# Optimization experiments

Hardware: AMD Instinct MI355X
Metric: run time of the kernel (lower is better)

Reference implementation:

```python
import jax, jax.numpy as jnp
import numpy as np
from jax import lax

B, T, D, H, HODE = 1024, 128, 64, 256, 256
DT = 0.1  # times spaced by 0.1 == integration_step_size -> one RK4 step per interval


def setup_inputs() -> dict:
    key = jax.random.key(0)
    ks = jax.random.split(key, 10)
    s = lambda fan: 1.0 / np.sqrt(fan)
    return {
        "x": jax.random.normal(ks[0], (B, T, D), jnp.float32),
        "times": jnp.arange(T, dtype=jnp.float32) * DT,
        "mask": (jax.random.uniform(ks[1], (B, T)) > 0.3).astype(jnp.float32),
        # ODE MLP: Linear(H->HODE), ReLU, Linear(HODE->H)
        "W1": jax.random.uniform(ks[2], (HODE, H), jnp.float32, -s(H), s(H)),
        "b1": jax.random.uniform(ks[3], (HODE,), jnp.float32, -s(H), s(H)),
        "W2": jax.random.uniform(ks[4], (H, HODE), jnp.float32, -s(HODE), s(HODE)),
        "b2": jax.random.uniform(ks[5], (H,), jnp.float32, -s(HODE), s(HODE)),
        # GRUCell params (torch layout: [3H, D]/[3H, H], gate order r,z,n)
        "W_ih": jax.random.uniform(ks[6], (3 * H, D), jnp.float32, -s(H), s(H)),
        "b_ih": jax.random.uniform(ks[7], (3 * H,), jnp.float32, -s(H), s(H)),
        "W_hh": jax.random.uniform(ks[8], (3 * H, H), jnp.float32, -s(H), s(H)),
        "b_hh": jax.random.uniform(ks[9], (3 * H,), jnp.float32, -s(H), s(H)),
    }


def _ode_gru_forward(x, times, mask, W1, b1, W2, b2, W_ih, b_ih, W_hh, b_hh):
    Bs, Ts, _ = x.shape
    Hs = W_hh.shape[1]

    def f(h):  # autonomous ODE vector field: MLP(h)
        return jnp.maximum(h @ W1.T + b1, 0.0) @ W2.T + b2

    def rk4_step(h, dt):
        k1 = f(h)
        k2 = f(h + 0.5 * dt * k1)
        k3 = f(h + 0.5 * dt * k2)
        k4 = f(h + dt * k3)
        return h + (dt / 6.0) * (k1 + 2.0 * k2 + 2.0 * k3 + k4)

    def gru_update(xt, h, m):
        gi = xt @ W_ih.T + b_ih  # [B, 3H]
        gh = h @ W_hh.T + b_hh
        i_r, i_z, i_n = jnp.split(gi, 3, axis=-1)
        h_r, h_z, h_n = jnp.split(gh, 3, axis=-1)
        r = jax.nn.sigmoid(i_r + h_r)
        z = jax.nn.sigmoid(i_z + h_z)
        n = jnp.tanh(i_n + r * h_n)
        h_next = (1.0 - z) * n + z * h
        m = m[:, None]
        return m * h_next + (1.0 - m) * h

    h0 = gru_update(x[:, 0], jnp.zeros((Bs, Hs), x.dtype), mask[:, 0])
    dts = times[1:] - times[:-1]  # [T-1]

    def step(h, inp):
        xt, mt, dt = inp
        h_ode = rk4_step(h, dt)
        h = gru_update(xt, h_ode, mt)
        return h, h

    xs = (jnp.swapaxes(x[:, 1:], 0, 1), jnp.swapaxes(mask[:, 1:], 0, 1), dts)
    _, hs = lax.scan(step, h0, xs)  # hs: [T-1, B, H]
    out = jnp.concatenate([h0[None], hs], axis=0)  # [T, B, H]
    return jnp.swapaxes(out, 0, 1)  # [B, T, H]


def reference(x, times, mask, W1, b1, W2, b2, W_ih, b_ih, W_hh, b_hh):
    return _ode_gru_forward(x, times, mask, W1, b1, W2, b2, W_ih, b_ih, W_hh, b_hh)
```

## Files before the change

kernel.cpp:

```cpp
#include <hip/hip_runtime.h>
#include <math.h>

#define BN 1024
#define TT 128
#define DD 64
#define HH 256
#define H3 768
#define BB 4

__device__ float g_W1t[HH * HH];
__device__ float g_W2t[HH * HH];
__device__ float g_Whht[HH * H3];
__device__ float g_Wiht[DD * H3];

__global__ __launch_bounds__(256) void prep_kernel(
    const float* __restrict__ W1, const float* __restrict__ W2,
    const float* __restrict__ Whh, const float* __restrict__ Wih)
{
  const int idx = blockIdx.x * blockDim.x + threadIdx.x;
  if (idx < HH * HH) {
    const int k = idx >> 8;
    const int i = idx & (HH - 1);
    g_W1t[idx] = W1[i * HH + k];
    g_W2t[idx] = W2[i * HH + k];
  }
  if (idx < HH * H3) {
    const int k = idx / H3;
    const int j = idx - k * H3;
    g_Whht[idx] = Whh[j * HH + k];
  }
  if (idx < DD * H3) {
    const int k = idx / H3;
    const int j = idx - k * H3;
    g_Wiht[idx] = Wih[j * DD + k];
  }
}

#define MV256(WT, INBUF, ACC) do {                                         \
    ACC[0] = 0.0f; ACC[1] = 0.0f; ACC[2] = 0.0f; ACC[3] = 0.0f;            \
    const float* wp_ = &(WT)[i];                                           \
    _Pragma("unroll 8")                                                    \
    for (int k_ = 0; k_ < HH; ++k_) {                                      \
      const float w_ = wp_[k_ * HH];                                       \
      const float4 hv_ = *reinterpret_cast<const float4*>(&(INBUF)[k_][0]);\
      ACC[0] = fmaf(w_, hv_.x, ACC[0]);                                    \
      ACC[1] = fmaf(w_, hv_.y, ACC[1]);                                    \
      ACC[2] = fmaf(w_, hv_.z, ACC[2]);                                    \
      ACC[3] = fmaf(w_, hv_.w, ACC[3]);                                    \
    }                                                                      \
  } while (0)

#define FEVAL(INBUF, KV) do {                                              \
    float a_[BB];                                                          \
    MV256(g_W1t, INBUF, a_);                                               \
    _Pragma("unroll")                                                      \
    for (int bb_ = 0; bb_ < BB; ++bb_)                                     \
      sh_u[i][bb_] = fmaxf(a_[bb_] + b1i, 0.0f);                           \
    __syncthreads();                                                       \
    MV256(g_W2t, sh_u, a_);                                                \
    _Pragma("unroll")                                                      \
    for (int bb_ = 0; bb_ < BB; ++bb_) KV[bb_] = a_[bb_] + b2i;            \
  } while (0)

__global__ __launch_bounds__(256) void odegru_kernel(
    const float* __restrict__ x, const float* __restrict__ times,
    const float* __restrict__ mask,
    const float* __restrict__ b1, const float* __restrict__ b2,
    const float* __restrict__ bih, const float* __restrict__ bhh,
    float* __restrict__ out)
{
  const int i = threadIdx.x;
  const int bbase = blockIdx.x * BB;

  __shared__ __align__(16) float sh_h[HH][BB];
  __shared__ __align__(16) float sh_in[HH][BB];
  __shared__ __align__(16) float sh_u[HH][BB];
  __shared__ __align__(16) float sh_x[DD][BB];

  const float b1i = b1[i];
  const float b2i = b2[i];
  const float bihr = bih[i], bihz = bih[i + HH], bihn = bih[i + 2 * HH];
  const float bhhr = bhh[i], bhhz = bhh[i + HH], bhhn = bhh[i + 2 * HH];

#pragma unroll
  for (int bb = 0; bb < BB; ++bb) sh_h[i][bb] = 0.0f;

  for (int t = 0; t < TT; ++t) {
    {
      const int bb = i >> 6, d = i & 63;
      sh_x[d][bb] = x[((size_t)(bbase + bb) * TT + t) * DD + d];
    }
    if (t == 0) {
#pragma unroll
      for (int bb = 0; bb < BB; ++bb) sh_in[i][bb] = 0.0f;
    }
    __syncthreads();

    if (t > 0) {
      const float dt = times[t] - times[t - 1];
      float kv[BB], ks[BB];

      FEVAL(sh_h, kv);
#pragma unroll
      for (int bb = 0; bb < BB; ++bb) {
        ks[bb] = kv[bb];
        sh_in[i][bb] = sh_h[i][bb] + 0.5f * dt * kv[bb];
      }
      __syncthreads();
      FEVAL(sh_in, kv);
#pragma unroll
      for (int bb = 0; bb < BB; ++bb) {
        ks[bb] += 2.0f * kv[bb];
        sh_in[i][bb] = sh_h[i][bb] + 0.5f * dt * kv[bb];
      }
      __syncthreads();
      FEVAL(sh_in, kv);
#pragma unroll
      for (int bb = 0; bb < BB; ++bb) {
        ks[bb] += 2.0f * kv[bb];
        sh_in[i][bb] = sh_h[i][bb] + dt * kv[bb];
      }
      __syncthreads();
      FEVAL(sh_in, kv);
#pragma unroll
      for (int bb = 0; bb < BB; ++bb) {
        ks[bb] += kv[bb];
        sh_in[i][bb] = sh_h[i][bb] + (dt * (1.0f / 6.0f)) * ks[bb];
      }
      __syncthreads();
    }

    float racc[BB], zacc[BB], ghn[BB], gin[BB];
#pragma unroll
    for (int bb = 0; bb < BB; ++bb) {
      racc[bb] = bihr + bhhr;
      zacc[bb] = bihz + bhhz;
      ghn[bb] = bhhn;
      gin[bb] = bihn;
    }

    {
      const float* wp = &g_Whht[i];
#pragma unroll 4
      for (int k = 0; k < HH; ++k) {
        const float4 hv = *reinterpret_cast<const float4*>(&sh_in[k][0]);
        const float wr = wp[k * H3];
        const float wz = wp[k * H3 + HH];
        const float wn = wp[k * H3 + 2 * HH];
        racc[0] = fmaf(wr, hv.x, racc[0]); racc[1] = fmaf(wr, hv.y, racc[1]);
        racc[2] = fmaf(wr, hv.z, racc[2]); racc[3] = fmaf(wr, hv.w, racc[3]);
        zacc[0] = fmaf(wz, hv.x, zacc[0]); zacc[1] = fmaf(wz, hv.y, zacc[1]);
        zacc[2] = fmaf(wz, hv.z, zacc[2]); zacc[3] = fmaf(wz, hv.w, zacc[3]);
        ghn[0] = fmaf(wn, hv.x, ghn[0]); ghn[1] = fmaf(wn, hv.y, ghn[1]);
        ghn[2] = fmaf(wn, hv.z, ghn[2]); ghn[3] = fmaf(wn, hv.w, ghn[3]);
      }
    }
    {
      const float* wp = &g_Wiht[i];
#pragma unroll 4
      for (int k = 0; k < DD; ++k) {
        const float4 xv = *reinterpret_cast<const float4*>(&sh_x[k][0]);
        const float wr = wp[k * H3];
        const float wz = wp[k * H3 + HH];
        const float wn = wp[k * H3 + 2 * HH];
        racc[0] = fmaf(wr, xv.x, racc[0]); racc[1] = fmaf(wr, xv.y, racc[1]);
        racc[2] = fmaf(wr, xv.z, racc[2]); racc[3] = fmaf(wr, xv.w, racc[3]);
        zacc[0] = fmaf(wz, xv.x, zacc[0]); zacc[1] = fmaf(wz, xv.y, zacc[1]);
        zacc[2] = fmaf(wz, xv.z, zacc[2]); zacc[3] = fmaf(wz, xv.w, zacc[3]);
        gin[0] = fmaf(wn, xv.x, gin[0]); gin[1] = fmaf(wn, xv.y, gin[1]);
        gin[2] = fmaf(wn, xv.z, gin[2]); gin[3] = fmaf(wn, xv.w, gin[3]);
      }
    }

#pragma unroll
    for (int bb = 0; bb < BB; ++bb) {
      const float r = 1.0f / (1.0f + expf(-racc[bb]));
      const float z = 1.0f / (1.0f + expf(-zacc[bb]));
      const float n = tanhf(gin[bb] + r * ghn[bb]);
      const float hode = sh_in[i][bb];
      const float hnext = (1.0f - z) * n + z * hode;
      const float m = mask[(size_t)(bbase + bb) * TT + t];
      const float hnew = m * hnext + (1.0f - m) * hode;
      out[((size_t)(bbase + bb) * TT + t) * HH + i] = hnew;
      sh_h[i][bb] = hnew;
    }
    __syncthreads();
  }
}

extern "C" void kernel_launch(void* const* d_in, const int* in_sizes, int n_in,
                              void* d_out, int out_size, void* d_ws, size_t ws_size,
                              hipStream_t stream) {
  (void)in_sizes; (void)n_in; (void)d_ws; (void)ws_size; (void)out_size;
  const float* x     = (const float*)d_in[0];
  const float* times = (const float*)d_in[1];
  const float* mask  = (const float*)d_in[2];
  const float* W1    = (const float*)d_in[3];
  const float* b1    = (const float*)d_in[4];
  const float* W2    = (const float*)d_in[5];
  const float* b2    = (const float*)d_in[6];
  const float* Wih   = (const float*)d_in[7];
  const float* bih   = (const float*)d_in[8];
  const float* Whh   = (const float*)d_in[9];
  const float* bhh   = (const float*)d_in[10];
  float* out = (float*)d_out;

  hipLaunchKernelGGL(prep_kernel, dim3((HH * H3 + 255) / 256), dim3(256), 0, stream,
                     W1, W2, Whh, Wih);
  hipLaunchKernelGGL(odegru_kernel, dim3(BN / BB), dim3(HH), 0, stream,
                     x, times, mask, b1, b2, bih, bhh, out);
}
```

Baseline: 7.415 ms.

## Rewrite ODE-GRU recurrence with split-bf16 MFMA and 16-row batch tiles

Replaces the scalar FMA matrix-vector loops with bf16 MFMA 16x16x32 instructions. Weights are pre-packed into fragment layout as hi/lo bf16 pairs, and activations are split on the fly, so three products approximate fp32 accuracy. Each block now handles 16 batch rows with 512 threads over 64 blocks. Gate pre-activations are staged in padded shared memory, and fast exp is used for sigmoid and tanh. The goal is to move the recurrent matmuls onto the matrix cores, at the cost of some precision loss and only 64 blocks, which leaves most CUs idle.

```diff
diff --git a/kernel.cpp b/kernel.cpp
--- a/kernel.cpp
+++ b/kernel.cpp
@@ -1,188 +1,345 @@
 #include <hip/hip_runtime.h>
 #include <math.h>
 
-#define BN 1024
-#define TT 128
+#define TT_ 128
 #define DD 64
 #define HH 256
-#define H3 768
-#define BB 4
-
-__device__ float g_W1t[HH * HH];
-__device__ float g_W2t[HH * HH];
-__device__ float g_Whht[HH * H3];
-__device__ float g_Wiht[DD * H3];
-
-__global__ __launch_bounds__(256) void prep_kernel(
+#define BB 16
+#define NBLK 64
+#define NTHR 512
+
+#define SA 260
+#define SX 68
+#define SG 516
+
+typedef short bf16x8 __attribute__((ext_vector_type(8)));
+typedef float f32x4 __attribute__((ext_vector_type(4)));
+typedef unsigned int uint;
+typedef unsigned short ushort;
+typedef uint u32x4 __attribute__((ext_vector_type(4)));
+
+__device__ ushort g_W1p[16 * 8 * 2 * 512];
+__device__ ushort g_W2p[16 * 8 * 2 * 512];
+__device__ ushort g_Wrzp[32 * 10 * 2 * 512];
+__device__ ushort g_Whnp[16 * 8 * 2 * 512];
+__device__ ushort g_Winp[16 * 2 * 512];
+
+__device__ __forceinline__ ushort bf16_rne(float f) {
+  uint u = __builtin_bit_cast(uint, f);
+  return (ushort)((u + 0x7fffu + ((u >> 16) & 1u)) >> 16);
+}
+__device__ __forceinline__ float bf16_f32(ushort h) {
+  uint u = ((uint)h) << 16;
+  return __builtin_bit_cast(float, u);
+}
+
+__global__ __launch_bounds__(256) void prep(
     const float* __restrict__ W1, const float* __restrict__ W2,
-    const float* __restrict__ Whh, const float* __restrict__ Wih)
-{
-  const int idx = blockIdx.x * blockDim.x + threadIdx.x;
-  if (idx < HH * HH) {
-    const int k = idx >> 8;
-    const int i = idx & (HH - 1);
-    g_W1t[idx] = W1[i * HH + k];
-    g_W2t[idx] = W2[i * HH + k];
-  }
-  if (idx < HH * H3) {
-    const int k = idx / H3;
-    const int j = idx - k * H3;
-    g_Whht[idx] = Whh[j * HH + k];
-  }
-  if (idx < DD * H3) {
-    const int k = idx / H3;
-    const int j = idx - k * H3;
-    g_Wiht[idx] = Wih[j * DD + k];
-  }
-}
-
-#define MV256(WT, INBUF, ACC) do {                                         \
-    ACC[0] = 0.0f; ACC[1] = 0.0f; ACC[2] = 0.0f; ACC[3] = 0.0f;            \
-    const float* wp_ = &(WT)[i];                                           \
-    _Pragma("unroll 8")                                                    \
-    for (int k_ = 0; k_ < HH; ++k_) {                                      \
-      const float w_ = wp_[k_ * HH];                                       \
-      const float4 hv_ = *reinterpret_cast<const float4*>(&(INBUF)[k_][0]);\
-      ACC[0] = fmaf(w_, hv_.x, ACC[0]);                                    \
-      ACC[1] = fmaf(w_, hv_.y, ACC[1]);                                    \
-      ACC[2] = fmaf(w_, hv_.z, ACC[2]);                                    \
-      ACC[3] = fmaf(w_, hv_.w, ACC[3]);                                    \
-    }                                                                      \
-  } while (0)
-
-#define FEVAL(INBUF, KV) do {                                              \
-    float a_[BB];                                                          \
-    MV256(g_W1t, INBUF, a_);                                               \
-    _Pragma("unroll")                                                      \
-    for (int bb_ = 0; bb_ < BB; ++bb_)                                     \
-      sh_u[i][bb_] = fmaxf(a_[bb_] + b1i, 0.0f);                           \
-    __syncthreads();                                                       \
-    MV256(g_W2t, sh_u, a_);                                                \
-    _Pragma("unroll")                                                      \
-    for (int bb_ = 0; bb_ < BB; ++bb_) KV[bb_] = a_[bb_] + b2i;            \
-  } while (0)
-
-__global__ __launch_bounds__(256) void odegru_kernel(
+    const float* __restrict__ Wih, const float* __restrict__ Whh)
+{
+  const int s = blockIdx.x * 256 + threadIdx.x;
+  const int S1 = 16 * 8 * 512;
+  const int S2 = S1 + 16 * 8 * 512;
+  const int S3 = S2 + 32 * 10 * 512;
+  const int S4 = S3 + 16 * 8 * 512;
+  const int S5 = S4 + 16 * 2 * 512;
+  if (s >= S5) return;
+
+  if (s < S2) {
+    const int r = (s < S1) ? s : s - S1;
+    const int t = r / (8 * 512);
+    const int o = (r / 512) & 7;
+    const int pos = r & 511;
+    const int l = pos >> 3, j = pos & 7;
+    const int n = t * 16 + (l & 15);
+    const int k = o * 32 + (l >> 4) * 8 + j;
+    const float w = (s < S1) ? W1[n * HH + k] : W2[n * HH + k];
+    ushort hi = bf16_rne(w);
+    ushort lo = bf16_rne(w - bf16_f32(hi));
+    ushort* dst = (s < S1) ? g_W1p : g_W2p;
+    dst[((t * 8 + o) * 2) * 512 + pos] = hi;
+    dst[((t * 8 + o) * 2 + 1) * 512 + pos] = lo;
+  } else if (s < S3) {
+    const int r = s - S2;
+    const int t = r / (10 * 512);
+    const int o = (r / 512) % 10;
+    const int pos = r & 511;
+    const int l = pos >> 3, j = pos & 7;
+    const int n = t * 16 + (l & 15);
+    float w;
+    if (o < 8) w = Whh[n * HH + o * 32 + (l >> 4) * 8 + j];
+    else       w = Wih[n * DD + (o - 8) * 32 + (l >> 4) * 8 + j];
+    ushort hi = bf16_rne(w);
+    ushort lo = bf16_rne(w - bf16_f32(hi));
+    g_Wrzp[((t * 10 + o) * 2) * 512 + pos] = hi;
+    g_Wrzp[((t * 10 + o) * 2 + 1) * 512 + pos] = lo;
+  } else if (s < S4) {
+    const int r = s - S3;
+    const int t = r / (8 * 512);
+    const int o = (r / 512) & 7;
+    const int pos = r & 511;
+    const int l = pos >> 3, j = pos & 7;
+    const int n = 512 + t * 16 + (l & 15);
+    const float w = Whh[n * HH + o * 32 + (l >> 4) * 8 + j];
+    ushort hi = bf16_rne(w);
+    ushort lo = bf16_rne(w - bf16_f32(hi));
+    g_Whnp[((t * 8 + o) * 2) * 512 + pos] = hi;
+    g_Whnp[((t * 8 + o) * 2 + 1) * 512 + pos] = lo;
+  } else {
+    const int r = s - S4;
+    const int t = r / (2 * 512);
+    const int o = (r / 512) & 1;
+    const int pos = r & 511;
+    const int l = pos >> 3, j = pos & 7;
+    const int n = 512 + t * 16 + (l & 15);
+    const float w = Wih[n * DD + o * 32 + (l >> 4) * 8 + j];
+    g_Winp[(t * 2 + o) * 512 + pos] = bf16_rne(w);
+  }
+}
+
+__device__ __forceinline__ void build_frags(const float* __restrict__ ap,
+                                            bf16x8& ahi, bf16x8& alo)
+{
+  const float4 a0 = *(const float4*)ap;
+  const float4 a1 = *(const float4*)(ap + 4);
+  float af[8] = {a0.x, a0.y, a0.z, a0.w, a1.x, a1.y, a1.z, a1.w};
+  uint hu[4], lu[4];
+#pragma unroll
+  for (int jj = 0; jj < 4; ++jj) {
+    const uint ue = __builtin_bit_cast(uint, af[2 * jj]);
+    const uint uo = __builtin_bit_cast(uint, af[2 * jj + 1]);
+    hu[jj] = (ue >> 16) | (uo & 0xffff0000u);
+    const float he = __builtin_bit_cast(float, ue & 0xffff0000u);
+    const float ho = __builtin_bit_cast(float, uo & 0xffff0000u);
+    const uint le = __builtin_bit_cast(uint, af[2 * jj] - he);
+    const uint lo = __builtin_bit_cast(uint, af[2 * jj + 1] - ho);
+    lu[jj] = (le >> 16) | (lo & 0xffff0000u);
+  }
+  u32x4 hv = {hu[0], hu[1], hu[2], hu[3]};
+  u32x4 lv = {lu[0], lu[1], lu[2], lu[3]};
+  ahi = __builtin_bit_cast(bf16x8, hv);
+  alo = __builtin_bit_cast(bf16x8, lv);
+}
+
+#define MFMA(A, B, C) __builtin_amdgcn_mfma_f32_16x16x32_bf16((A), (B), (C), 0, 0, 0)
+
+__device__ __forceinline__ void mm2t3(const float* __restrict__ src, int stride,
+                                      const ushort* __restrict__ pack, int t0,
+                                      int lane, f32x4& acc0, f32x4& acc1)
+{
+  const int l15 = lane & 15, lq = lane >> 4;
+  const ushort* pb = pack + lane * 8;
+#pragma unroll
+  for (int o = 0; o < 8; ++o) {
+    bf16x8 ahi, alo;
+    build_frags(src + l15 * stride + o * 32 + lq * 8, ahi, alo);
+    const ushort* p0 = pb + ((t0 * 8 + o) * 2) * 512;
+    const ushort* p1 = pb + (((t0 + 1) * 8 + o) * 2) * 512;
+    const bf16x8 w0h = *(const bf16x8*)p0;
+    const bf16x8 w0l = *(const bf16x8*)(p0 + 512);
+    const bf16x8 w1h = *(const bf16x8*)p1;
+    const bf16x8 w1l = *(const bf16x8*)(p1 + 512);
+    acc0 = MFMA(ahi, w0h, acc0);
+    acc1 = MFMA(ahi, w1h, acc1);
+    acc0 = MFMA(alo, w0h, acc0);
+    acc1 = MFMA(alo, w1h, acc1);
+    acc0 = MFMA(ahi, w0l, acc0);
+    acc1 = MFMA(ahi, w1l, acc1);
+  }
+}
+
+__device__ __forceinline__ void mm_rz(const float* __restrict__ hsrc,
+                                      const float* __restrict__ xsrc,
+                                      int lane, int w, f32x4 az[4])
+{
+  const int l15 = lane & 15, lq = lane >> 4;
+  const ushort* pb = g_Wrzp + lane * 8;
+#pragma unroll
+  for (int o = 0; o < 8; ++o) {
+    bf16x8 ahi, alo;
+    build_frags(hsrc + l15 * SA + o * 32 + lq * 8, ahi, alo);
+#pragma unroll
+    for (int q = 0; q < 4; ++q) {
+      const int t = 4 * w + q;
+      const ushort* p = pb + ((t * 10 + o) * 2) * 512;
+      const bf16x8 wh = *(const bf16x8*)p;
+      const bf16x8 wl = *(const bf16x8*)(p + 512);
+      az[q] = MFMA(ahi, wh, az[q]);
+      az[q] = MFMA(alo, wh, az[q]);
+      az[q] = MFMA(ahi, wl, az[q]);
+    }
+  }
+#pragma unroll
+  for (int o = 0; o < 2; ++o) {
+    bf16x8 ahi, alo;
+    build_frags(xsrc + l15 * SX + o * 32 + lq * 8, ahi, alo);
+#pragma unroll
+    for (int q = 0; q < 4; ++q) {
+      const int t = 4 * w + q;
+      const ushort* p = pb + ((t * 10 + 8 + o) * 2) * 512;
+      const bf16x8 wh = *(const bf16x8*)p;
+      az[q] = MFMA(ahi, wh, az[q]);
+      az[q] = MFMA(alo, wh, az[q]);
+    }
+  }
+}
+
+__device__ __forceinline__ void mm_in_f(const float* __restrict__ xsrc,
+                                        int lane, int t0, f32x4& acc0, f32x4& acc1)
+{
+  const int l15 = lane & 15, lq = lane >> 4;
+#pragma unroll
+  for (int o = 0; o < 2; ++o) {
+    bf16x8 ahi, alo;
+    build_frags(xsrc + l15 * SX + o * 32 + lq * 8, ahi, alo);
+    const bf16x8 w0 = *(const bf16x8*)(g_Winp + (t0 * 2 + o) * 512 + lane * 8);
+    const bf16x8 w1 = *(const bf16x8*)(g_Winp + ((t0 + 1) * 2 + o) * 512 + lane * 8);
+    acc0 = MFMA(ahi, w0, acc0);
+    acc0 = MFMA(alo, w0, acc0);
+    acc1 = MFMA(ahi, w1, acc1);
+    acc1 = MFMA(alo, w1, acc1);
+  }
+}
+
+__global__ __launch_bounds__(NTHR, 2) void odegru_kernel(
     const float* __restrict__ x, const float* __restrict__ times,
     const float* __restrict__ mask,
     const float* __restrict__ b1, const float* __restrict__ b2,
     const float* __restrict__ bih, const float* __restrict__ bhh,
     float* __restrict__ out)
 {
-  const int i = threadIdx.x;
-  const int bbase = blockIdx.x * BB;
-
-  __shared__ __align__(16) float sh_h[HH][BB];
-  __shared__ __align__(16) float sh_in[HH][BB];
-  __shared__ __align__(16) float sh_u[HH][BB];
-  __shared__ __align__(16) float sh_x[DD][BB];
-
-  const float b1i = b1[i];
-  const float b2i = b2[i];
-  const float bihr = bih[i], bihz = bih[i + HH], bihn = bih[i + 2 * HH];
-  const float bhhr = bhh[i], bhhz = bhh[i + HH], bhhn = bhh[i + 2 * HH];
-
-#pragma unroll
-  for (int bb = 0; bb < BB; ++bb) sh_h[i][bb] = 0.0f;
-
-  for (int t = 0; t < TT; ++t) {
+  __shared__ __align__(16) float sAh[BB * SA];
+  __shared__ __align__(16) float sAin[BB * SA];
+  __shared__ __align__(16) float sU[BB * SA];
+  __shared__ __align__(16) float sX[BB * SX];
+  __shared__ __align__(16) float sGRZ[BB * SG];
+  __shared__ __align__(16) float sGHN[BB * SA];
+  __shared__ __align__(16) float sGIN[BB * SA];
+
+  const int tid = threadIdx.x;
+  const int lane = tid & 63;
+  const int w = tid >> 6;
+  const int l15 = lane & 15;
+  const int lq = lane >> 4;
+  const int b0 = blockIdx.x * BB;
+
+  const int c0 = (2 * w) * 16 + l15;
+  const int c1 = (2 * w + 1) * 16 + l15;
+  const float b1c0 = b1[c0], b1c1 = b1[c1];
+  const float b2c0 = b2[c0], b2c1 = b2[c1];
+
+  const int pi = tid & 255;
+  const int pb0 = (tid >> 8) * 8;
+  const float brz_r = bih[pi] + bhh[pi];
+  const float brz_z = bih[pi + 256] + bhh[pi + 256];
+  const float bn_i = bih[pi + 512];
+  const float bn_h = bhh[pi + 512];
+
+  const f32x4 Z = {0.f, 0.f, 0.f, 0.f};
+
+  auto feval = [&](const float* src, f32x4& kv0, f32x4& kv1) {
+    f32x4 a0 = Z, a1 = Z;
+    mm2t3(src, SA, g_W1p, 2 * w, lane, a0, a1);
+#pragma unroll
+    for (int r = 0; r < 4; ++r) {
+      const int b = lq * 4 + r;
+      sU[b * SA + c0] = fmaxf(a0[r] + b1c0, 0.f);
+      sU[b * SA + c1] = fmaxf(a1[r] + b1c1, 0.f);
+    }
+    __syncthreads();
+    f32x4 p0 = Z, p1 = Z;
+    mm2t3(sU, SA, g_W2p, 2 * w, lane, p0, p1);
+    kv0 = p0 + b2c0;
+    kv1 = p1 + b2c1;
+  };
+
+  auto wAin = [&](float coef, const f32x4& v0, const f32x4& v1) {
+#pragma unroll
+    for (int r = 0; r < 4; ++r) {
+      const int b = lq * 4 + r;
+      sAin[b * SA + c0] = sAh[b * SA + c0] + coef * v0[r];
+      sAin[b * SA + c1] = sAh[b * SA + c1] + coef * v1[r];
+    }
+  };
+
+  for (int t = 0; t < TT_; ++t) {
     {
-      const int bb = i >> 6, d = i & 63;
-      sh_x[d][bb] = x[((size_t)(bbase + bb) * TT + t) * DD + d];
+      const int b = tid >> 5, d = (tid & 31) * 2;
+      const float2 v = *(const float2*)&x[((size_t)(b0 + b) * TT_ + t) * DD + d];
+      sX[b * SX + d] = v.x;
+      sX[b * SX + d + 1] = v.y;
     }
     if (t == 0) {
 #pragma unroll
-      for (int bb = 0; bb < BB; ++bb) sh_in[i][bb] = 0.0f;
+      for (int q = 0; q < 8; ++q) {
+        const int idx = tid * 8 + q;
+        sAin[(idx >> 8) * SA + (idx & 255)] = 0.f;
+      }
     }
     __syncthreads();
 
     if (t > 0) {
-      const float dt = times[t] - times[t - 1];
-      float kv[BB], ks[BB];
-
-      FEVAL(sh_h, kv);
-#pragma unroll
-      for (int bb = 0; bb < BB; ++bb) {
-        ks[bb] = kv[bb];
-        sh_in[i][bb] = sh_h[i][bb] + 0.5f * dt * kv[bb];
+      const float dtv = times[t] - times[t - 1];
+      f32x4 kv0, kv1, ks0, ks1;
+      feval(sAh, kv0, kv1);
+      ks0 = kv0; ks1 = kv1;
+      wAin(0.5f * dtv, kv0, kv1);
+      __syncthreads();
+      feval(sAin, kv0, kv1);
+      ks0 += 2.0f * kv0; ks1 += 2.0f * kv1;
+      wAin(0.5f * dtv, kv0, kv1);
+      __syncthreads();
+      feval(sAin, kv0, kv1);
+      ks0 += 2.0f * kv0; ks1 += 2.0f * kv1;
+      wAin(dtv, kv0, kv1);
+      __syncthreads();
+      feval(sAin, kv0, kv1);
+      ks0 += kv0; ks1 += kv1;
+      wAin(dtv * (1.0f / 6.0f), ks0, ks1);
+      __syncthreads();
+    }
+
+    {
+      f32x4 az[4] = {Z, Z, Z, Z};
+      mm_rz(sAin, sX, lane, w, az);
+#pragma unroll
+      for (int q = 0; q < 4; ++q)
+#pragma unroll
+        for (int r = 0; r < 4; ++r) {
+          const int b = lq * 4 + r;
+          sGRZ[b * SG + (4 * w + q) * 16 + l15] = az[q][r];
+        }
+      f32x4 h0 = Z, h1 = Z;
+      mm2t3(sAin, SA, g_Whnp, 2 * w, lane, h0, h1);
+      f32x4 i0 = Z, i1 = Z;
+      mm_in_f(sX, lane, 2 * w, i0, i1);
+#pragma unroll
+      for (int r = 0; r < 4; ++r) {
+        const int b = lq * 4 + r;
+        sGHN[b * SA + c0] = h0[r];
+        sGHN[b * SA + c1] = h1[r];
+        sGIN[b * SA + c0] = i0[r];
+        sGIN[b * SA + c1] = i1[r];
       }
-      __syncthreads();
-      FEVAL(sh_in, kv);
-#pragma unroll
-      for (int bb = 0; bb < BB; ++bb) {
-        ks[bb] += 2.0f * kv[bb];
-        sh_in[i][bb] = sh_h[i][bb] + 0.5f * dt * kv[bb];
-      }
-      __syncthreads();
-      FEVAL(sh_in, kv);
-#pragma unroll
-      for (int bb = 0; bb < BB; ++bb) {
-        ks[bb] += 2.0f * kv[bb];
-        sh_in[i][bb] = sh_h[i][bb] + dt * kv[bb];
-      }
-      __syncthreads();
-      FEVAL(sh_in, kv);
-#pragma unroll
-      for (int bb = 0; bb < BB; ++bb) {
-        ks[bb] += kv[bb];
-        sh_in[i][bb] = sh_h[i][bb] + (dt * (1.0f / 6.0f)) * ks[bb];
-      }
-      __syncthreads();
-    }
-
-    float racc[BB], zacc[BB], ghn[BB], gin[BB];
-#pragma unroll
-    for (int bb = 0; bb < BB; ++bb) {
-      racc[bb] = bihr + bhhr;
-      zacc[bb] = bihz + bhhz;
-      ghn[bb] = bhhn;
-      gin[bb] = bihn;
-    }
-
-    {
-      const float* wp = &g_Whht[i];
-#pragma unroll 4
-      for (int k = 0; k < HH; ++k) {
-        const float4 hv = *reinterpret_cast<const float4*>(&sh_in[k][0]);
-        const float wr = wp[k * H3];
-        const float wz = wp[k * H3 + HH];
-        const float wn = wp[k * H3 + 2 * HH];
-        racc[0] = fmaf(wr, hv.x, racc[0]); racc[1] = fmaf(wr, hv.y, racc[1]);
-        racc[2] = fmaf(wr, hv.z, racc[2]); racc[3] = fmaf(wr, hv.w, racc[3]);
-        zacc[0] = fmaf(wz, hv.x, zacc[0]); zacc[1] = fmaf(wz, hv.y, zacc[1]);
-        zacc[2] = fmaf(wz, hv.z, zacc[2]); zacc[3] = fmaf(wz, hv.w, zacc[3]);
-        ghn[0] = fmaf(wn, hv.x, ghn[0]); ghn[1] = fmaf(wn, hv.y, ghn[1]);
-        ghn[2] = fmaf(wn, hv.z, ghn[2]); ghn[3] = fmaf(wn, hv.w, ghn[3]);
-      }
-    }
-    {
-      const float* wp = &g_Wiht[i];
-#pragma unroll 4
-      for (int k = 0; k < DD; ++k) {
-        const float4 xv = *reinterpret_cast<const float4*>(&sh_x[k][0]);
-        const float wr = wp[k * H3];
-        const float wz = wp[k * H3 + HH];
-        const float wn = wp[k * H3 + 2 * HH];
-        racc[0] = fmaf(wr, xv.x, racc[0]); racc[1] = fmaf(wr, xv.y, racc[1]);
-        racc[2] = fmaf(wr, xv.z, racc[2]); racc[3] = fmaf(wr, xv.w, racc[3]);
-        zacc[0] = fmaf(wz, xv.x, zacc[0]); zacc[1] = fmaf(wz, xv.y, zacc[1]);
-        zacc[2] = fmaf(wz, xv.z, zacc[2]); zacc[3] = fmaf(wz, xv.w, zacc[3]);
-        gin[0] = fmaf(wn, xv.x, gin[0]); gin[1] = fmaf(wn, xv.y, gin[1]);
-        gin[2] = fmaf(wn, xv.z, gin[2]); gin[3] = fmaf(wn, xv.w, gin[3]);
-      }
-    }
-
-#pragma unroll
-    for (int bb = 0; bb < BB; ++bb) {
-      const float r = 1.0f / (1.0f + expf(-racc[bb]));
-      const float z = 1.0f / (1.0f + expf(-zacc[bb]));
-      const float n = tanhf(gin[bb] + r * ghn[bb]);
-      const float hode = sh_in[i][bb];
-      const float hnext = (1.0f - z) * n + z * hode;
-      const float m = mask[(size_t)(bbase + bb) * TT + t];
-      const float hnew = m * hnext + (1.0f - m) * hode;
-      out[((size_t)(bbase + bb) * TT + t) * HH + i] = hnew;
-      sh_h[i][bb] = hnew;
+    }
+    __syncthreads();
+
+#pragma unroll
+    for (int bb = 0; bb < 8; ++bb) {
+      const int b = pb0 + bb;
+      const float gr = sGRZ[b * SG + pi] + brz_r;
+      const float gz = sGRZ[b * SG + pi + 256] + brz_z;
+      const float hn = sGHN[b * SA + pi] + bn_h;
+      const float gn = sGIN[b * SA + pi] + bn_i;
+      const float hode = sAin[b * SA + pi];
+      const float rg = 1.f / (1.f + __expf(-gr));
+      const float zg = 1.f / (1.f + __expf(-gz));
+      const float ng = 1.f - 2.f / (__expf(2.f * (gn + rg * hn)) + 1.f);
+      const float hnext = (1.f - zg) * ng + zg * hode;
+      const float m = mask[(size_t)(b0 + b) * TT_ + t];
+      const float hnew = m * hnext + (1.f - m) * hode;
+      sAh[b * SA + pi] = hnew;
+      out[((size_t)(b0 + b) * TT_ + t) * HH + pi] = hnew;
     }
     __syncthreads();
   }
@@ -205,8 +362,8 @@
   const float* bhh   = (const float*)d_in[10];
   float* out = (float*)d_out;
 
-  hipLaunchKernelGGL(prep_kernel, dim3((HH * H3 + 255) / 256), dim3(256), 0, stream,
-                     W1, W2, Whh, Wih);
-  hipLaunchKernelGGL(odegru_kernel, dim3(BN / BB), dim3(HH), 0, stream,
+  hipLaunchKernelGGL(prep, dim3((376832 + 255) / 256), dim3(256), 0, stream,
+                     W1, W2, Wih, Whh);
+  hipLaunchKernelGGL(odegru_kernel, dim3(NBLK), dim3(NTHR), 0, stream,
                      x, times, mask, b1, b2, bih, bhh, out);
 }
```

Result: no change. 7.528 ms (+1.5%).
